# Optimization experiments

Hardware: AMD Instinct MI355X
Metric: run time of the kernel (lower is better)

The kernel has to match this reference:

```python
import jax, jax.numpy as jnp
import numpy as np

THRESH = 0.7  # TWN-style threshold factor: delta = 0.7 * mean|W|


def ternarize(W):
    """Quantize latent float weights to alpha * {-1, 0, +1} (per-tensor scale)."""
    absW = jnp.abs(W)
    delta = THRESH * jnp.mean(absW)
    mask = (absW > delta).astype(W.dtype)
    n = jnp.maximum(jnp.sum(mask), 1.0)
    alpha = jnp.sum(absW * mask) / n
    return alpha * jnp.sign(W) * mask


def setup_inputs() -> dict:
    key = jax.random.key(0)
    k_x, k_w1, k_b1, k_w2, k_b2 = jax.random.split(key, 5)
    B = 65536
    x = jax.random.normal(k_x, (B, 784), dtype=jnp.float32)
    # latent float weights (torch Linear layout: [out, in]), kaiming-ish scale
    W1 = jax.random.normal(k_w1, (64, 784), dtype=jnp.float32) * (1.0 / np.sqrt(784))
    b1 = jax.random.normal(k_b1, (64,), dtype=jnp.float32) * 0.01
    W2 = jax.random.normal(k_w2, (10, 64), dtype=jnp.float32) * (1.0 / np.sqrt(64))
    b2 = jax.random.normal(k_b2, (10,), dtype=jnp.float32) * 0.01
    return {"x": x, "W1": W1, "b1": b1, "W2": W2, "b2": b2}


def reference(x, W1, b1, W2, b2):
    x = x.reshape(-1, 784)
    Wq1 = ternarize(W1)  # [64, 784]
    Wq2 = ternarize(W2)  # [10, 64]
    h = jax.nn.relu(x @ Wq1.T + b1)   # [B, 64]
    out = h @ Wq2.T + b2              # [B, 10]
    return out
```

## Files before the change

### kernel.cpp

```cpp
#include <hip/hip_runtime.h>
#include <hip/hip_bf16.h>


typedef __attribute__((ext_vector_type(4))) float f32x4;
typedef __attribute__((ext_vector_type(8))) short s16x8;
typedef __attribute__((ext_vector_type(4))) unsigned int u32x4;

#define K1 784
#define K1_PAD 800
#define NHID 64
#define NOUT 10

static __device__ __forceinline__ unsigned short f2bf_rne(float f) {
    unsigned int u = __builtin_bit_cast(unsigned int, f);
    unsigned int r = u + 0x7FFFu + ((u >> 16) & 1u);
    return (unsigned short)(r >> 16);
}

static __device__ __forceinline__ unsigned int cvt_pk_bf16(float lo, float hi) {
    unsigned int r;
    asm("v_cvt_pk_bf16_f32 %0, %1, %2" : "=v"(r) : "v"(lo), "v"(hi));
    return r;
}

static __device__ double block_sum256(double v, double* red) {
    #pragma unroll
    for (int off = 32; off > 0; off >>= 1) v += __shfl_down(v, off, 64);
    const int w = threadIdx.x >> 6;
    const int lane = threadIdx.x & 63;
    __syncthreads();
    if (lane == 0) red[w] = v;
    __syncthreads();
    return red[0] + red[1] + red[2] + red[3];
}


__global__ __launch_bounds__(256) void tern_sum_kernel(
    const float* __restrict__ W1, const float* __restrict__ W2,
    double* __restrict__ p1, double* __restrict__ p2)
{
    __shared__ double red[4];
    const int gid = blockIdx.x * 256 + threadIdx.x;

    double s = 0.0;
    if (gid < (NHID * K1) / 4) {
        f32x4 v = ((const f32x4*)W1)[gid];
        s = (double)fabsf(v[0]) + (double)fabsf(v[1])
          + (double)fabsf(v[2]) + (double)fabsf(v[3]);
    }
    s = block_sum256(s, red);
    if (threadIdx.x == 0) p1[blockIdx.x] = s;

    if (blockIdx.x == 0) {
        double s2 = 0.0;
        if (threadIdx.x < (NOUT * NHID) / 4) {
            f32x4 v = ((const f32x4*)W2)[threadIdx.x];
            s2 = (double)fabsf(v[0]) + (double)fabsf(v[1])
               + (double)fabsf(v[2]) + (double)fabsf(v[3]);
        }
        s2 = block_sum256(s2, red);
        if (threadIdx.x == 0) p2[0] = s2;
    }
}

__global__ __launch_bounds__(256) void tern_quant_kernel(
    const float* __restrict__ W1, const float* __restrict__ W2,
    unsigned short* __restrict__ W1q, unsigned short* __restrict__ W2q,
    const double* __restrict__ p1, const double* __restrict__ p2,
    double* __restrict__ psm, double* __restrict__ pcn,
    double* __restrict__ a2)
{
    __shared__ double red[4];

    double v = (threadIdx.x < 64) ? p1[threadIdx.x] : 0.0;
    const double s1 = block_sum256(v, red);
    const float delta1 = (float)(0.7 * s1 / (double)(NHID * K1));

    const int n = blockIdx.x;
    double sm = 0.0, cn = 0.0;
    for (int k = threadIdx.x; k < K1_PAD; k += 256) {
        unsigned short q = 0;
        if (k < K1) {
            float w = W1[n * K1 + k];
            float a = fabsf(w);
            if (a > delta1) { q = (w > 0.0f) ? 0x3F80u : 0xBF80u; sm += (double)a; cn += 1.0; }
        }
        W1q[n * K1_PAD + k] = q;
    }
    sm = block_sum256(sm, red);
    cn = block_sum256(cn, red);
    if (threadIdx.x == 0) { psm[n] = sm; pcn[n] = cn; }

    if (blockIdx.x == 0) {
        const float delta2 = (float)(0.7 * p2[0] / (double)(NOUT * NHID));
        double sm2 = 0.0, cn2 = 0.0;
        for (int i = threadIdx.x; i < 16 * NHID; i += 256) {
            int r = i >> 6;
            int k = i & 63;
            unsigned short q = 0;
            if (r < NOUT) {
                float w = W2[r * NHID + k];
                float a = fabsf(w);
                if (a > delta2) { q = (w > 0.0f) ? 0x3F80u : 0xBF80u; sm2 += (double)a; cn2 += 1.0; }
            }
            W2q[i] = q;
        }
        sm2 = block_sum256(sm2, red);
        cn2 = block_sum256(cn2, red);
        if (threadIdx.x == 0) a2[0] = sm2 / fmax(cn2, 1.0);
    }
}

__global__ __launch_bounds__(256) void fused_kernel(
    const float* __restrict__ x,
    const float* __restrict__ b1,
    const float* __restrict__ b2,
    const short* __restrict__ W1q,
    const short* __restrict__ W2q,
    const double* __restrict__ psm,
    const double* __restrict__ pcn,
    const double* __restrict__ a2,
    float* __restrict__ out)
{
    const int tid  = threadIdx.x;
    const int wave = tid >> 6;
    const int lane = tid & 63;
    const int low  = lane & 15;
    const int quad = lane >> 4;

    const int m0 = blockIdx.x * 64 + wave * 16;

    const float* ga = x + (size_t)(m0 + low) * K1 + quad * 8;

    __shared__ __align__(16) unsigned short h_lds[4][16][72];

    const short* wbase = W1q + (size_t)low * K1_PAD + quad * 8;

    f32x4 acc[4];
    #pragma unroll
    for (int nt = 0; nt < 4; ++nt) acc[nt] = (f32x4){0.f, 0.f, 0.f, 0.f};

    const f32x4 zero4 = (f32x4){0.f, 0.f, 0.f, 0.f};

    f32x4 c0 = *(const f32x4*)(ga);
    f32x4 c1 = *(const f32x4*)(ga + 4);
    s16x8 bf[4];
    #pragma unroll
    for (int nt = 0; nt < 4; ++nt)
        bf[nt] = *(const s16x8*)(wbase + (size_t)nt * 16 * K1_PAD);

    for (int ks = 0; ks < 25; ++ks) {
        f32x4 n0 = zero4, n1 = zero4;
        s16x8 bn[4];
        if (ks < 24) {
            const short* wn = wbase + (ks + 1) * 32;
            #pragma unroll
            for (int nt = 0; nt < 4; ++nt)
                bn[nt] = *(const s16x8*)(wn + (size_t)nt * 16 * K1_PAD);
            const int kf = (ks + 1) * 32 + quad * 8;
            if (kf < K1) {
                n0 = *(const f32x4*)(ga + (ks + 1) * 32);
                n1 = *(const f32x4*)(ga + (ks + 1) * 32 + 4);
            }
        }

        u32x4 au;
        au[0] = cvt_pk_bf16(c0[0], c0[1]);
        au[1] = cvt_pk_bf16(c0[2], c0[3]);
        au[2] = cvt_pk_bf16(c1[0], c1[1]);
        au[3] = cvt_pk_bf16(c1[2], c1[3]);
        s16x8 a = __builtin_bit_cast(s16x8, au);

        #pragma unroll
        for (int nt = 0; nt < 4; ++nt)
            acc[nt] = __builtin_amdgcn_mfma_f32_16x16x32_bf16(a, bf[nt], acc[nt], 0, 0, 0);

        #pragma unroll
        for (int nt = 0; nt < 4; ++nt) bf[nt] = bn[nt];
        c0 = n0; c1 = n1;
    }

    double vs = psm[lane], vc = pcn[lane];
    #pragma unroll
    for (int off = 32; off > 0; off >>= 1) {
        vs += __shfl_down(vs, off, 64);
        vc += __shfl_down(vc, off, 64);
    }
    vs = __shfl(vs, 0, 64);
    vc = __shfl(vc, 0, 64);
    const float alpha1 = (float)(vs / fmax(vc, 1.0));
    const float alpha2 = (float)a2[0];

    #pragma unroll
    for (int nt = 0; nt < 4; ++nt) {
        const int n = nt * 16 + low;
        const float bias = b1[n];
        #pragma unroll
        for (int r = 0; r < 4; ++r) {
            float hv = fmaxf(0.0f, fmaf(alpha1, acc[nt][r], bias));
            h_lds[wave][quad * 4 + r][n] = f2bf_rne(hv);
        }
    }
    __asm__ volatile("s_waitcnt lgkmcnt(0)" ::: "memory");

    s16x8 a0 = *(const s16x8*)(&h_lds[wave][low][quad * 8]);
    s16x8 a1 = *(const s16x8*)(&h_lds[wave][low][32 + quad * 8]);
    s16x8 w0 = *(const s16x8*)(W2q + low * 64 + quad * 8);
    s16x8 w1 = *(const s16x8*)(W2q + low * 64 + 32 + quad * 8);

    f32x4 acc2 = (f32x4){0.f, 0.f, 0.f, 0.f};
    acc2 = __builtin_amdgcn_mfma_f32_16x16x32_bf16(a0, w0, acc2, 0, 0, 0);
    acc2 = __builtin_amdgcn_mfma_f32_16x16x32_bf16(a1, w1, acc2, 0, 0, 0);

    if (low < NOUT) {
        const float bias2 = b2[low];
        #pragma unroll
        for (int r = 0; r < 4; ++r) {
            const int row = m0 + quad * 4 + r;
            out[(size_t)row * NOUT + low] = fmaf(alpha2, acc2[r], bias2);
        }
    }
}

extern "C" void kernel_launch(void* const* d_in, const int* in_sizes, int n_in,
                              void* d_out, int out_size, void* d_ws, size_t ws_size,
                              hipStream_t stream) {
    const float* x  = (const float*)d_in[0];
    const float* W1 = (const float*)d_in[1];
    const float* b1 = (const float*)d_in[2];
    const float* W2 = (const float*)d_in[3];
    const float* b2 = (const float*)d_in[4];
    float* out = (float*)d_out;

    const int nrows = in_sizes[0] / K1;

    char* base = (char*)d_ws;
    double* p1  = (double*)(base);
    double* psm = (double*)(base + 512);
    double* pcn = (double*)(base + 1024);
    double* p2  = (double*)(base + 1536);
    double* a2  = (double*)(base + 1544);
    unsigned short* W1q = (unsigned short*)(base + 2048);
    unsigned short* W2q = W1q + NHID * K1_PAD;

    tern_sum_kernel<<<64, 256, 0, stream>>>(W1, W2, p1, p2);
    tern_quant_kernel<<<64, 256, 0, stream>>>(W1, W2, W1q, W2q, p1, p2, psm, pcn, a2);

    const int nblocks = nrows / 64;
    fused_kernel<<<nblocks, 256, 0, stream>>>(x, b1, b2, (const short*)W1q,
                                              (const short*)W2q, psm, pcn, a2, out);
}
```

Before: 318.2 us.

## Merge ternarization kernels and deepen x prefetch to two steps ahead

The two weight-ternarization kernels are merged into one: each of the 64 blocks recomputes the full mean|W1| reduction itself instead of reading per-block partials from a prior launch. This removes one kernel launch and its dependency gap at the cost of redundant reads of W1 per block. The main GEMM loop is fully unrolled, and x loads are now issued two K-steps ahead instead of one to hide more global memory latency. This raises register pressure from the extra buffers.

```diff
diff --git a/kernel.cpp b/kernel.cpp
--- a/kernel.cpp
+++ b/kernel.cpp
@@ -10,6 +10,7 @@
 #define K1_PAD 800
 #define NHID 64
 #define NOUT 10
+#define NSTEP 25
 
 static __device__ __forceinline__ unsigned short f2bf_rne(float f) {
     unsigned int u = __builtin_bit_cast(unsigned int, f);
@@ -34,51 +35,27 @@
     return red[0] + red[1] + red[2] + red[3];
 }
 
-
-__global__ __launch_bounds__(256) void tern_sum_kernel(
-    const float* __restrict__ W1, const float* __restrict__ W2,
-    double* __restrict__ p1, double* __restrict__ p2)
-{
-    __shared__ double red[4];
-    const int gid = blockIdx.x * 256 + threadIdx.x;
-
-    double s = 0.0;
-    if (gid < (NHID * K1) / 4) {
-        f32x4 v = ((const f32x4*)W1)[gid];
-        s = (double)fabsf(v[0]) + (double)fabsf(v[1])
-          + (double)fabsf(v[2]) + (double)fabsf(v[3]);
-    }
-    s = block_sum256(s, red);
-    if (threadIdx.x == 0) p1[blockIdx.x] = s;
-
-    if (blockIdx.x == 0) {
-        double s2 = 0.0;
-        if (threadIdx.x < (NOUT * NHID) / 4) {
-            f32x4 v = ((const f32x4*)W2)[threadIdx.x];
-            s2 = (double)fabsf(v[0]) + (double)fabsf(v[1])
-               + (double)fabsf(v[2]) + (double)fabsf(v[3]);
-        }
-        s2 = block_sum256(s2, red);
-        if (threadIdx.x == 0) p2[0] = s2;
-    }
-}
-
-__global__ __launch_bounds__(256) void tern_quant_kernel(
+__global__ __launch_bounds__(256) void tern_all_kernel(
     const float* __restrict__ W1, const float* __restrict__ W2,
     unsigned short* __restrict__ W1q, unsigned short* __restrict__ W2q,
-    const double* __restrict__ p1, const double* __restrict__ p2,
     double* __restrict__ psm, double* __restrict__ pcn,
     double* __restrict__ a2)
 {
     __shared__ double red[4];
-
-    double v = (threadIdx.x < 64) ? p1[threadIdx.x] : 0.0;
-    const double s1 = block_sum256(v, red);
-    const float delta1 = (float)(0.7 * s1 / (double)(NHID * K1));
+    const int tid = threadIdx.x;
+
+    double s = 0.0;
+    for (int i = tid; i < (NHID * K1) / 4; i += 256) {
+        f32x4 v = ((const f32x4*)W1)[i];
+        s += (double)fabsf(v[0]) + (double)fabsf(v[1])
+           + (double)fabsf(v[2]) + (double)fabsf(v[3]);
+    }
+    s = block_sum256(s, red);
+    const float delta1 = (float)(0.7 * s / (double)(NHID * K1));
 
     const int n = blockIdx.x;
     double sm = 0.0, cn = 0.0;
-    for (int k = threadIdx.x; k < K1_PAD; k += 256) {
+    for (int k = tid; k < K1_PAD; k += 256) {
         unsigned short q = 0;
         if (k < K1) {
             float w = W1[n * K1 + k];
@@ -89,12 +66,20 @@
     }
     sm = block_sum256(sm, red);
     cn = block_sum256(cn, red);
-    if (threadIdx.x == 0) { psm[n] = sm; pcn[n] = cn; }
+    if (tid == 0) { psm[n] = sm; pcn[n] = cn; }
 
     if (blockIdx.x == 0) {
-        const float delta2 = (float)(0.7 * p2[0] / (double)(NOUT * NHID));
+        double s2 = 0.0;
+        if (tid < (NOUT * NHID) / 4) {
+            f32x4 v = ((const f32x4*)W2)[tid];
+            s2 = (double)fabsf(v[0]) + (double)fabsf(v[1])
+               + (double)fabsf(v[2]) + (double)fabsf(v[3]);
+        }
+        s2 = block_sum256(s2, red);
+        const float delta2 = (float)(0.7 * s2 / (double)(NOUT * NHID));
+
         double sm2 = 0.0, cn2 = 0.0;
-        for (int i = threadIdx.x; i < 16 * NHID; i += 256) {
+        for (int i = tid; i < 16 * NHID; i += 256) {
             int r = i >> 6;
             int k = i & 63;
             unsigned short q = 0;
@@ -107,7 +92,7 @@
         }
         sm2 = block_sum256(sm2, red);
         cn2 = block_sum256(cn2, red);
-        if (threadIdx.x == 0) a2[0] = sm2 / fmax(cn2, 1.0);
+        if (tid == 0) a2[0] = sm2 / fmax(cn2, 1.0);
     }
 }
 
@@ -142,33 +127,42 @@
 
     const f32x4 zero4 = (f32x4){0.f, 0.f, 0.f, 0.f};
 
-    f32x4 c0 = *(const f32x4*)(ga);
-    f32x4 c1 = *(const f32x4*)(ga + 4);
-    s16x8 bf[4];
+    f32x4 cA0 = *(const f32x4*)(ga);
+    f32x4 cA1 = *(const f32x4*)(ga + 4);
+    f32x4 cB0 = *(const f32x4*)(ga + 32);
+    f32x4 cB1 = *(const f32x4*)(ga + 36);
+    f32x4 cC0, cC1;
+
+    s16x8 bf[4], bn[4];
     #pragma unroll
     for (int nt = 0; nt < 4; ++nt)
         bf[nt] = *(const s16x8*)(wbase + (size_t)nt * 16 * K1_PAD);
 
-    for (int ks = 0; ks < 25; ++ks) {
-        f32x4 n0 = zero4, n1 = zero4;
-        s16x8 bn[4];
-        if (ks < 24) {
+    #pragma unroll
+    for (int ks = 0; ks < NSTEP; ++ks) {
+        if (ks + 2 < NSTEP) {
+            const int kf = (ks + 2) * 32 + quad * 8;
+            if (kf < K1) {
+                cC0 = *(const f32x4*)(ga + (ks + 2) * 32);
+                cC1 = *(const f32x4*)(ga + (ks + 2) * 32 + 4);
+            } else {
+                cC0 = zero4; cC1 = zero4;
+            }
+        } else {
+            cC0 = zero4; cC1 = zero4;
+        }
+        if (ks + 1 < NSTEP) {
             const short* wn = wbase + (ks + 1) * 32;
             #pragma unroll
             for (int nt = 0; nt < 4; ++nt)
                 bn[nt] = *(const s16x8*)(wn + (size_t)nt * 16 * K1_PAD);
-            const int kf = (ks + 1) * 32 + quad * 8;
-            if (kf < K1) {
-                n0 = *(const f32x4*)(ga + (ks + 1) * 32);
-                n1 = *(const f32x4*)(ga + (ks + 1) * 32 + 4);
-            }
         }
 
         u32x4 au;
-        au[0] = cvt_pk_bf16(c0[0], c0[1]);
-        au[1] = cvt_pk_bf16(c0[2], c0[3]);
-        au[2] = cvt_pk_bf16(c1[0], c1[1]);
-        au[3] = cvt_pk_bf16(c1[2], c1[3]);
+        au[0] = cvt_pk_bf16(cA0[0], cA0[1]);
+        au[1] = cvt_pk_bf16(cA0[2], cA0[3]);
+        au[2] = cvt_pk_bf16(cA1[0], cA1[1]);
+        au[3] = cvt_pk_bf16(cA1[2], cA1[3]);
         s16x8 a = __builtin_bit_cast(s16x8, au);
 
         #pragma unroll
@@ -177,7 +171,7 @@
 
         #pragma unroll
         for (int nt = 0; nt < 4; ++nt) bf[nt] = bn[nt];
-        c0 = n0; c1 = n1;
+        cA0 = cB0; cA1 = cB1; cB0 = cC0; cB1 = cC1;
     }
 
     double vs = psm[lane], vc = pcn[lane];
@@ -235,16 +229,13 @@
     const int nrows = in_sizes[0] / K1;
 
     char* base = (char*)d_ws;
-    double* p1  = (double*)(base);
-    double* psm = (double*)(base + 512);
-    double* pcn = (double*)(base + 1024);
-    double* p2  = (double*)(base + 1536);
-    double* a2  = (double*)(base + 1544);
-    unsigned short* W1q = (unsigned short*)(base + 2048);
+    double* psm = (double*)(base);
+    double* pcn = (double*)(base + 512);
+    double* a2  = (double*)(base + 1024);
+    unsigned short* W1q = (unsigned short*)(base + 1088);
     unsigned short* W2q = W1q + NHID * K1_PAD;
 
-    tern_sum_kernel<<<64, 256, 0, stream>>>(W1, W2, p1, p2);
-    tern_quant_kernel<<<64, 256, 0, stream>>>(W1, W2, W1q, W2q, p1, p2, psm, pcn, a2);
+    tern_all_kernel<<<64, 256, 0, stream>>>(W1, W2, W1q, W2q, psm, pcn, a2);
 
     const int nblocks = nrows / 64;
     fused_kernel<<<nblocks, 256, 0, stream>>>(x, b1, b2, (const short*)W1q,
```

Result: slower. 338.6 us (+6.4%).
